# Performance work log

Measured on AMD Instinct MI355X. Metric: run time of the kernel, lower is better.

The kernel has to match this reference:

```python
import jax, jax.numpy as jnp
import numpy as np


def setup_inputs() -> dict:
    key = jax.random.key(0)
    k1, k2, k3 = jax.random.split(key, 3)
    B, P, N, D = 128, 4096, 64, 2
    batch = jax.random.uniform(k1, (B, P, D), dtype=jnp.float32)
    not_dummy_points = jnp.ones((B, P), dtype=jnp.float32)
    centers = jax.random.uniform(k2, (N, D), dtype=jnp.float32)
    sharpness = jnp.ones((N, D), dtype=jnp.float32) * 3.0
    return {"batch": batch, "not_dummy_points": not_dummy_points,
            "centers": centers, "sharpness": sharpness}


def reference(batch, not_dummy_points, centers, sharpness):
    # batch: [B,P,D], not_dummy_points: [B,P], centers/sharpness: [N,D]
    # diff[b,n,p,d] = centers[n,d] - batch[b,p,d]
    diff = centers[None, :, None, :] - batch[:, None, :, :]        # [B,N,P,D]
    # weighted squared distance, sharpness squared per original
    dist = jnp.sum(diff * diff * (sharpness ** 2)[None, :, None, :], axis=-1)  # [B,N,P]
    x = jnp.exp(-dist) * not_dummy_points[:, None, :]              # mask dummy points
    return jnp.sum(x, axis=-1)                                     # [B,N]
```

## Files before the change

kernel.cpp:

```cpp
#include <hip/hip_runtime.h>


constexpr int B_ = 128;
constexpr int P_ = 4096;
constexpr int N_ = 64;
constexpr int CPB = 16;
constexpr int THREADS = 256;
constexpr int WAVES = THREADS / 64;
constexpr int PTS_PER_BLOCK = P_ / CPB;
constexpr int PTS_PER_WAVE  = PTS_PER_BLOCK / WAVES;

#if __has_builtin(__builtin_amdgcn_exp2f)
#define EXP2(x) __builtin_amdgcn_exp2f(x)
#else
#define EXP2(x) exp2f(x)
#endif

static __device__ __forceinline__ float rdlane(float v, int l) {
    return __int_as_float(__builtin_amdgcn_readlane(__float_as_int(v), l));
}

__global__ __launch_bounds__(THREADS, 8) void slayer_stage1(
    const float* __restrict__ batch,
    const float* __restrict__ ndp,
    const float* __restrict__ centers,
    const float* __restrict__ sharp,
    float* __restrict__ partial)
{
    const int tid  = threadIdx.x;
    const int lane = tid & 63;
    const int wave = tid >> 6;
    const int b     = blockIdx.x / CPB;
    const int chunk = blockIdx.x % CPB;
    const int p0 = chunk * PTS_PER_BLOCK + wave * PTS_PER_WAVE;

    const float2 q = reinterpret_cast<const float2*>(batch)[(size_t)b * P_ + p0 + lane];
    const float  m = ndp[(size_t)b * P_ + p0 + lane];
    float px = q.x, py = q.y;
    if (m == 0.f) { px = 1e18f; py = 1e18f; }

    const float2 cc = reinterpret_cast<const float2*>(centers)[lane];
    const float2 ss = reinterpret_cast<const float2*>(sharp)[lane];
    constexpr float LOG2E = 1.44269504088896340736f;
    const float w0 = ss.x * ss.x * LOG2E;
    const float w1 = ss.y * ss.y * LOG2E;
    const float A0 = -w0,           A1 = -w1;
    const float B0 = 2.f*w0*cc.x,   B1 = 2.f*w1*cc.y;
    const float E  = -(w0*cc.x*cc.x + w1*cc.y*cc.y);

    float acc0 = 0.f, acc1 = 0.f;
    #pragma unroll
    for (int i = 0; i < PTS_PER_WAVE; i += 2) {
        const float x0 = rdlane(px, i),     y0 = rdlane(py, i);
        const float x1 = rdlane(px, i + 1), y1 = rdlane(py, i + 1);

        float t0 = fmaf(A0, x0, B0), t1 = fmaf(A1, y0, B1);
        float u0 = fmaf(t0, x0, E);  u0 = fmaf(t1, y0, u0);

        float r0 = fmaf(A0, x1, B0), r1 = fmaf(A1, y1, B1);
        float u1 = fmaf(r0, x1, E);  u1 = fmaf(r1, y1, u1);

        acc0 += EXP2(u0);
        acc1 += EXP2(u1);
    }

    __shared__ float red[THREADS];
    red[tid] = acc0 + acc1;
    __syncthreads();
    if (tid < 64) {
        partial[(size_t)blockIdx.x * N_ + tid] =
            red[tid] + red[tid + 64] + red[tid + 128] + red[tid + 192];
    }
}

__global__ __launch_bounds__(256) void slayer_stage2(
    const float* __restrict__ partial,
    float* __restrict__ out)
{
    const int idx = blockIdx.x * 256 + threadIdx.x;
    const int b = idx >> 6;
    const int n = idx & 63;
    const float* p = partial + (size_t)b * CPB * N_ + n;
    float s = 0.f;
    #pragma unroll
    for (int c = 0; c < CPB; ++c) s += p[c * N_];
    out[idx] = s;
}

extern "C" void kernel_launch(void* const* d_in, const int* in_sizes, int n_in,
                              void* d_out, int out_size, void* d_ws, size_t ws_size,
                              hipStream_t stream) {
    const float* batch   = (const float*)d_in[0];
    const float* ndp     = (const float*)d_in[1];
    const float* centers = (const float*)d_in[2];
    const float* sharp   = (const float*)d_in[3];
    float* out     = (float*)d_out;
    float* partial = (float*)d_ws;

    slayer_stage1<<<dim3(B_ * CPB), THREADS, 0, stream>>>(batch, ndp, centers, sharp, partial);
    slayer_stage2<<<dim3((B_ * N_) / 256), 256, 0, stream>>>(partial, out);
}
```

Measured before the change: 69.46 us.

## Fuse two-stage reduction into one kernel with threads over points

Replaces the two-kernel scheme with a single kernel. In the old first stage each lane owned a center and points were broadcast with readlane; the second stage summed the partials. Now each block owns one batch row and a group of 8 centers. Each thread streams float4 point pairs and keeps 8 accumulators, which are reduced with wave shuffles and a small shared-memory step and written straight to the output. This drops the second launch, the partial buffer and the readlane broadcasts, at the cost of re-reading each batch row once per center group and higher register use per thread.

Result: slower. 73.26 us (+5.5%).

```diff
diff --git a/kernel.cpp b/kernel.cpp
--- a/kernel.cpp
+++ b/kernel.cpp
@@ -4,11 +4,10 @@
 constexpr int B_ = 128;
 constexpr int P_ = 4096;
 constexpr int N_ = 64;
-constexpr int CPB = 16;
+constexpr int NG = 8;
+constexpr int GPB = N_ / NG;
 constexpr int THREADS = 256;
-constexpr int WAVES = THREADS / 64;
-constexpr int PTS_PER_BLOCK = P_ / CPB;
-constexpr int PTS_PER_WAVE  = PTS_PER_BLOCK / WAVES;
+constexpr int ITERS = P_ / (2 * THREADS);
 
 #if __has_builtin(__builtin_amdgcn_exp2f)
 #define EXP2(x) __builtin_amdgcn_exp2f(x)
@@ -16,75 +15,78 @@
 #define EXP2(x) exp2f(x)
 #endif
 
-static __device__ __forceinline__ float rdlane(float v, int l) {
-    return __int_as_float(__builtin_amdgcn_readlane(__float_as_int(v), l));
-}
-
-__global__ __launch_bounds__(THREADS, 8) void slayer_stage1(
+__global__ __launch_bounds__(THREADS, 4) void slayer_fused(
     const float* __restrict__ batch,
     const float* __restrict__ ndp,
     const float* __restrict__ centers,
     const float* __restrict__ sharp,
-    float* __restrict__ partial)
+    float* __restrict__ out)
 {
     const int tid  = threadIdx.x;
     const int lane = tid & 63;
     const int wave = tid >> 6;
-    const int b     = blockIdx.x / CPB;
-    const int chunk = blockIdx.x % CPB;
-    const int p0 = chunk * PTS_PER_BLOCK + wave * PTS_PER_WAVE;
+    const int b  = blockIdx.x / GPB;
+    const int g  = blockIdx.x % GPB;
+    const int n0 = g * NG;
 
-    const float2 q = reinterpret_cast<const float2*>(batch)[(size_t)b * P_ + p0 + lane];
-    const float  m = ndp[(size_t)b * P_ + p0 + lane];
-    float px = q.x, py = q.y;
-    if (m == 0.f) { px = 1e18f; py = 1e18f; }
-
-    const float2 cc = reinterpret_cast<const float2*>(centers)[lane];
-    const float2 ss = reinterpret_cast<const float2*>(sharp)[lane];
     constexpr float LOG2E = 1.44269504088896340736f;
-    const float w0 = ss.x * ss.x * LOG2E;
-    const float w1 = ss.y * ss.y * LOG2E;
-    const float A0 = -w0,           A1 = -w1;
-    const float B0 = 2.f*w0*cc.x,   B1 = 2.f*w1*cc.y;
-    const float E  = -(w0*cc.x*cc.x + w1*cc.y*cc.y);
-
-    float acc0 = 0.f, acc1 = 0.f;
+    float A0[NG], A1[NG], B0[NG], B1[NG], E[NG];
     #pragma unroll
-    for (int i = 0; i < PTS_PER_WAVE; i += 2) {
-        const float x0 = rdlane(px, i),     y0 = rdlane(py, i);
-        const float x1 = rdlane(px, i + 1), y1 = rdlane(py, i + 1);
-
-        float t0 = fmaf(A0, x0, B0), t1 = fmaf(A1, y0, B1);
-        float u0 = fmaf(t0, x0, E);  u0 = fmaf(t1, y0, u0);
-
-        float r0 = fmaf(A0, x1, B0), r1 = fmaf(A1, y1, B1);
-        float u1 = fmaf(r0, x1, E);  u1 = fmaf(r1, y1, u1);
-
-        acc0 += EXP2(u0);
-        acc1 += EXP2(u1);
+    for (int k = 0; k < NG; ++k) {
+        const float2 cc = reinterpret_cast<const float2*>(centers)[n0 + k];
+        const float2 ss = reinterpret_cast<const float2*>(sharp)[n0 + k];
+        const float w0 = ss.x * ss.x * LOG2E;
+        const float w1 = ss.y * ss.y * LOG2E;
+        A0[k] = -w0;            A1[k] = -w1;
+        B0[k] = 2.f*w0*cc.x;    B1[k] = 2.f*w1*cc.y;
+        E[k]  = -(w0*cc.x*cc.x + w1*cc.y*cc.y);
     }
 
-    __shared__ float red[THREADS];
-    red[tid] = acc0 + acc1;
+    float acc[NG];
+    #pragma unroll
+    for (int k = 0; k < NG; ++k) acc[k] = 0.f;
+
+    const float4* bp = reinterpret_cast<const float4*>(batch + (size_t)b * P_ * 2);
+    const float2* mp = reinterpret_cast<const float2*>(ndp + (size_t)b * P_);
+
+    #pragma unroll
+    for (int i = 0; i < ITERS; ++i) {
+        const float4 q = bp[i * THREADS + tid];
+        const float2 m = mp[i * THREADS + tid];
+        #pragma unroll
+        for (int k = 0; k < NG; ++k) {
+            float t0 = fmaf(A0[k], q.x, B0[k]);
+            float t1 = fmaf(A1[k], q.y, B1[k]);
+            float u  = fmaf(t0, q.x, E[k]);
+            u        = fmaf(t1, q.y, u);
+            float r0 = fmaf(A0[k], q.z, B0[k]);
+            float r1 = fmaf(A1[k], q.w, B1[k]);
+            float v  = fmaf(r0, q.z, E[k]);
+            v        = fmaf(r1, q.w, v);
+            acc[k] = fmaf(EXP2(u), m.x, acc[k]);
+            acc[k] = fmaf(EXP2(v), m.y, acc[k]);
+        }
+    }
+
+    #pragma unroll
+    for (int k = 0; k < NG; ++k) {
+        float v = acc[k];
+        #pragma unroll
+        for (int off = 32; off >= 1; off >>= 1)
+            v += __shfl_xor(v, off, 64);
+        acc[k] = v;
+    }
+
+    __shared__ float red[4][NG];
+    if (lane == 0) {
+        #pragma unroll
+        for (int k = 0; k < NG; ++k) red[wave][k] = acc[k];
+    }
     __syncthreads();
-    if (tid < 64) {
-        partial[(size_t)blockIdx.x * N_ + tid] =
-            red[tid] + red[tid + 64] + red[tid + 128] + red[tid + 192];
+    if (tid < NG) {
+        out[(size_t)b * N_ + n0 + tid] =
+            red[0][tid] + red[1][tid] + red[2][tid] + red[3][tid];
     }
-}
-
-__global__ __launch_bounds__(256) void slayer_stage2(
-    const float* __restrict__ partial,
-    float* __restrict__ out)
-{
-    const int idx = blockIdx.x * 256 + threadIdx.x;
-    const int b = idx >> 6;
-    const int n = idx & 63;
-    const float* p = partial + (size_t)b * CPB * N_ + n;
-    float s = 0.f;
-    #pragma unroll
-    for (int c = 0; c < CPB; ++c) s += p[c * N_];
-    out[idx] = s;
 }
 
 extern "C" void kernel_launch(void* const* d_in, const int* in_sizes, int n_in,
@@ -94,9 +96,8 @@
     const float* ndp     = (const float*)d_in[1];
     const float* centers = (const float*)d_in[2];
     const float* sharp   = (const float*)d_in[3];
-    float* out     = (float*)d_out;
-    float* partial = (float*)d_ws;
+    float* out = (float*)d_out;
+    (void)d_ws; (void)ws_size;
 
-    slayer_stage1<<<dim3(B_ * CPB), THREADS, 0, stream>>>(batch, ndp, centers, sharp, partial);
-    slayer_stage2<<<dim3((B_ * N_) / 256), 256, 0, stream>>>(partial, out);
+    slayer_fused<<<dim3(B_ * GPB), THREADS, 0, stream>>>(batch, ndp, centers, sharp, out);
 }
```
